# Kernel optimization log

Hardware: AMD Instinct MI355X
Metric: run time of the kernel (lower is better)

## Reference

```python
import jax, jax.numpy as jnp
import numpy as np

# dims
S = 8192       # total ragged tokens
B = 8          # number of sequences
L = 1024       # tokens per sequence (equal-length ragged batch)
HID = 2048     # hidden_size
H = 16         # num_attention_heads
KV = 4         # num_key_value_heads (GQA)
D = 128        # head_dim
HALF = D // 2
MAXPOS = 1024  # rope table length
MROPE_SECTION = [16, 24, 24]  # sums to HALF
SCALE = (1.0 / D) ** 0.5      # module default: sqrt(1/head_dim)
THETA = 1_000_000.0


def setup_inputs() -> dict:
    key = jax.random.key(0)
    ks = jax.random.split(key, 9)
    x = jax.random.normal(ks[0], (S, HID), jnp.float32)
    # torch-style Linear weights: [out_dim, in_dim]
    wq = jax.random.normal(ks[1], (H * D, HID), jnp.float32) * 0.02
    wk = jax.random.normal(ks[2], (KV * D, HID), jnp.float32) * 0.02
    wv = jax.random.normal(ks[3], (KV * D, HID), jnp.float32) * 0.02
    bq = jax.random.normal(ks[4], (H * D,), jnp.float32) * 0.02
    bk = jax.random.normal(ks[5], (KV * D,), jnp.float32) * 0.02
    bv = jax.random.normal(ks[6], (KV * D,), jnp.float32) * 0.02
    wo = jax.random.normal(ks[7], (HID, H * D), jnp.float32) * 0.02
    # rope table: freqs_cis[p, f] = (cos(p*inv_freq[f]), sin(p*inv_freq[f]))
    inv_freq = 1.0 / (THETA ** (jnp.arange(0, HALF, dtype=jnp.float32) / HALF))
    freqs = jnp.arange(MAXPOS, dtype=jnp.float32)[:, None] * inv_freq[None, :]
    freqs_cis = jnp.stack([jnp.cos(freqs), jnp.sin(freqs)], axis=-1)  # [MAXPOS, HALF, 2]
    # multi-axis (t/h/w) position ids, one row per mrope axis
    position_ids = jnp.tile(jnp.arange(L, dtype=jnp.int32), B)[None, :].repeat(3, axis=0)  # [3, S]
    input_row_offsets = jnp.arange(B + 1, dtype=jnp.int32) * L  # ragged offsets
    return {"x": x, "wq": wq, "wk": wk, "wv": wv, "bq": bq, "bk": bk, "bv": bv,
            "wo": wo, "freqs_cis": freqs_cis, "position_ids": position_ids,
            "input_row_offsets": input_row_offsets}


def _mrope_cos_sin(freqs_cis, position_ids):
    # gather per-axis cos/sin then select mrope sections along the freq dim
    cs = freqs_cis[position_ids]           # [3, S, HALF, 2]
    bounds = np.cumsum([0] + MROPE_SECTION)
    sel = jnp.concatenate([cs[i, :, bounds[i]:bounds[i + 1], :] for i in range(3)], axis=1)  # [S, HALF, 2]
    cos = sel[:, None, :, 0]               # [S, 1, HALF] broadcast over heads
    sin = sel[:, None, :, 1]
    return cos, sin


def _rope(t, cos, sin):
    # non-interleaved (rotate-half) rope on last dim of size D
    t1, t2 = jnp.split(t, 2, axis=-1)
    return jnp.concatenate([t1 * cos - t2 * sin, t2 * cos + t1 * sin], axis=-1)


def reference(x, wq, wk, wv, bq, bk, bv, wo, freqs_cis, position_ids, input_row_offsets):
    # fused ragged QKV projection (wqkv = concat(wq, wk, wv) along out dim)
    wqkv = jnp.concatenate([wq, wk, wv], axis=0)          # [H*D + 2*KV*D, HID]
    bqkv = jnp.concatenate([bq, bk, bv], axis=0)
    qkv = x @ wqkv.T + bqkv                                # [S, H*D + 2*KV*D]
    q = qkv[:, :H * D].reshape(S, H, D)
    k = qkv[:, H * D:H * D + KV * D].reshape(S, KV, D)
    v = qkv[:, H * D + KV * D:].reshape(S, KV, D)
    # fused multi-axis rotary embedding on q and k
    cos, sin = _mrope_cos_sin(freqs_cis, position_ids)
    q = _rope(q, cos, sin)
    k = _rope(k, cos, sin)
    # ragged causal flash attention; sequences are equal length so reshape to
    # [B, L, ...] which honors the ragged structure given input_row_offsets = arange(B+1)*L
    qb = q.reshape(B, L, H, D)
    kb = jnp.repeat(k.reshape(B, L, KV, D), H // KV, axis=2)  # GQA expand
    vb = jnp.repeat(v.reshape(B, L, KV, D), H // KV, axis=2)
    scores = jnp.einsum('bqhd,bkhd->bhqk', qb, kb) * SCALE    # [B, H, L, L]
    causal = jnp.tril(jnp.ones((L, L), dtype=bool))
    scores = jnp.where(causal, scores, jnp.float32(-1e30))
    attn = jax.nn.softmax(scores, axis=-1)
    out = jnp.einsum('bhqk,bkhd->bqhd', attn, vb).reshape(S, H * D)
    return out @ wo.T                                         # [S, HID]
```

## Files before the change

### kernel.cpp

```cpp
#include <hip/hip_runtime.h>

#define S_TOK 8192
#define BATCH 8
#define LSEQ 1024
#define HID 2048
#define NH 16
#define NKV 4
#define DHEAD 128
#define QKV_W 3072
#define SCALE_F 0.08838834764831845f

typedef __attribute__((ext_vector_type(8))) unsigned short u16x8;
typedef __attribute__((ext_vector_type(8))) __bf16 bf16x8;
typedef __attribute__((ext_vector_type(4))) float f32x4;

__device__ __forceinline__ unsigned short f2bf(float f) {
  unsigned u = __builtin_bit_cast(unsigned, f);
  unsigned r = u + 0x7fffu + ((u >> 16) & 1u);
  return (unsigned short)(r >> 16);
}
__device__ __forceinline__ float bf2f(unsigned short h) {
  return __builtin_bit_cast(float, (unsigned)h << 16);
}

__device__ __forceinline__ void async16(const void* g, void* l) {
  __builtin_amdgcn_global_load_lds(
      (const __attribute__((address_space(1))) void*)g,
      (__attribute__((address_space(3))) void*)l, 16, 0, 0);
}

__global__ __launch_bounds__(256) void conv_f2b(const float* __restrict__ src,
                                                unsigned short* __restrict__ dst,
                                                int n8) {
  int t = blockIdx.x * 256 + threadIdx.x;
  if (t >= n8) return;
  const f32x4* s4 = (const f32x4*)(src + (size_t)t * 8);
  f32x4 v0 = s4[0], v1 = s4[1];
  u16x8 o;
#pragma unroll
  for (int j = 0; j < 4; ++j) { o[j] = f2bf(v0[j]); o[4 + j] = f2bf(v1[j]); }
  *(u16x8*)(dst + (size_t)t * 8) = o;
}

__global__ __launch_bounds__(256) void conv_w3(const float* __restrict__ wq,
                                               const float* __restrict__ wk,
                                               const float* __restrict__ wv,
                                               unsigned short* __restrict__ dst,
                                               int n8) {
  int t = blockIdx.x * 256 + threadIdx.x;
  if (t >= n8) return;
  size_t idx = (size_t)t * 8;
  int row = (int)(idx >> 11);
  int col = (int)(idx & 2047);
  const float* src;
  if (row < 2048)      src = wq + ((size_t)row << 11) + col;
  else if (row < 2560) src = wk + ((size_t)(row - 2048) << 11) + col;
  else                 src = wv + ((size_t)(row - 2560) << 11) + col;
  const f32x4* s4 = (const f32x4*)src;
  f32x4 v0 = s4[0], v1 = s4[1];
  u16x8 o;
#pragma unroll
  for (int j = 0; j < 4; ++j) { o[j] = f2bf(v0[j]); o[4 + j] = f2bf(v1[j]); }
  *(u16x8*)(dst + idx) = o;
}

template <bool ADD_BIAS, bool OUT_BF16>
__global__ __launch_bounds__(256) void gemm_bt(const unsigned short* __restrict__ A,
                                               const unsigned short* __restrict__ Bw,
                                               const float* __restrict__ bias,
                                               void* __restrict__ Cout,
                                               int M, int N, int K) {
  __shared__ unsigned short A_lds[128 * 32];
  __shared__ unsigned short B_lds[128 * 32];
  const int tid = threadIdx.x;
  const int w = tid >> 6, lane = tid & 63;
  const int lr = lane & 15, lg = lane >> 4;
  const int wr = w >> 1, wc = w & 1;
  const int m0 = blockIdx.y * 128, n0 = blockIdx.x * 128;

  f32x4 acc[4][4];
#pragma unroll
  for (int mi = 0; mi < 4; ++mi)
#pragma unroll
    for (int nj = 0; nj < 4; ++nj) acc[mi][nj] = (f32x4){0.f, 0.f, 0.f, 0.f};

  const int nk = K >> 5;
  const int srow = (lane >> 2);
  const int scol = (lane & 3) * 8;
  for (int kt = 0; kt < nk; ++kt) {
#pragma unroll
    for (int q = 0; q < 2; ++q) {
      int chunk = w * 2 + q;
      int row = chunk * 16 + srow;
      async16(A + (size_t)(m0 + row) * K + kt * 32 + scol, &A_lds[chunk * 512]);
      async16(Bw + (size_t)(n0 + row) * K + kt * 32 + scol, &B_lds[chunk * 512]);
    }
    __syncthreads();
    bf16x8 a[4], bb[4];
#pragma unroll
    for (int mi = 0; mi < 4; ++mi)
      a[mi] = *(const bf16x8*)&A_lds[(wr * 64 + mi * 16 + lr) * 32 + lg * 8];
#pragma unroll
    for (int nj = 0; nj < 4; ++nj)
      bb[nj] = *(const bf16x8*)&B_lds[(wc * 64 + nj * 16 + lr) * 32 + lg * 8];
#pragma unroll
    for (int mi = 0; mi < 4; ++mi)
#pragma unroll
      for (int nj = 0; nj < 4; ++nj)
        acc[mi][nj] = __builtin_amdgcn_mfma_f32_16x16x32_bf16(a[mi], bb[nj], acc[mi][nj], 0, 0, 0);
    __syncthreads();
  }

#pragma unroll
  for (int mi = 0; mi < 4; ++mi)
#pragma unroll
    for (int nj = 0; nj < 4; ++nj)
#pragma unroll
      for (int j = 0; j < 4; ++j) {
        int row = m0 + wr * 64 + mi * 16 + lg * 4 + j;
        int col = n0 + wc * 64 + nj * 16 + lr;
        float v = acc[mi][nj][j];
        if (ADD_BIAS) v += bias[col];
        if (OUT_BF16)
          ((unsigned short*)Cout)[(size_t)row * N + col] = f2bf(v);
        else
          ((float*)Cout)[(size_t)row * N + col] = v;
      }
}

__global__ __launch_bounds__(256) void rope_k(unsigned short* __restrict__ qkv,
                                              const float* __restrict__ fc,
                                              const int* __restrict__ pid) {
  int t = blockIdx.x * 256 + threadIdx.x;
  int j0 = (t & 7) << 3;
  int hh = (t >> 3) % 20;
  int s = t / 160;
  if (s >= S_TOK) return;
  int sec = (j0 < 16) ? 0 : (j0 < 40 ? 1 : 2);
  int pos = pid[sec * S_TOK + s];
  const float* cs = fc + ((size_t)pos * 64 + j0) * 2;
  unsigned short* p = qkv + (size_t)s * QKV_W + hh * 128 + j0;
  u16x8 t1 = *(const u16x8*)p;
  u16x8 t2 = *(const u16x8*)(p + 64);
  u16x8 o1, o2;
#pragma unroll
  for (int j = 0; j < 8; ++j) {
    float c = cs[2 * j], sn = cs[2 * j + 1];
    float x1 = bf2f(t1[j]), x2 = bf2f(t2[j]);
    o1[j] = f2bf(x1 * c - x2 * sn);
    o2[j] = f2bf(x2 * c + x1 * sn);
  }
  *(u16x8*)p = o1;
  *(u16x8*)(p + 64) = o2;
}

__global__ __launch_bounds__(256) void attn_fwd(const unsigned short* __restrict__ qkv,
                                                unsigned short* __restrict__ aout) {
  __shared__ unsigned short K_lds[64 * 128];
  __shared__ unsigned short V_T[128 * 64];
  __shared__ unsigned short P_lds[4 * 32 * 64];
  char* Kb = (char*)K_lds;
  char* Vb = (char*)V_T;
  char* Pb = (char*)P_lds;
  const int tid = threadIdx.x, w = tid >> 6, lane = tid & 63;
  const int lr = lane & 15, lg = lane >> 4;
  const int q0 = blockIdx.x * 128, h = blockIdx.y, b = blockIdx.z, kvh = h >> 2;

  bf16x8 qf[2][4];
#pragma unroll
  for (int mi = 0; mi < 2; ++mi)
#pragma unroll
    for (int kk = 0; kk < 4; ++kk)
      qf[mi][kk] = *(const bf16x8*)(qkv + (size_t)(b * LSEQ + q0 + w * 32 + mi * 16 + lr) * QKV_W +
                                    h * 128 + kk * 32 + lg * 8);

  f32x4 o[2][8];
#pragma unroll
  for (int mi = 0; mi < 2; ++mi)
#pragma unroll
    for (int nj = 0; nj < 8; ++nj) o[mi][nj] = (f32x4){0.f, 0.f, 0.f, 0.f};
  float m_run[2][4], l_run[2][4];
#pragma unroll
  for (int mi = 0; mi < 2; ++mi)
#pragma unroll
    for (int j = 0; j < 4; ++j) { m_run[mi][j] = -1e30f; l_run[mi][j] = 0.f; }

  const int ntiles = (q0 >> 6) + 2;
  for (int kt = 0; kt < ntiles; ++kt) {
    const int k0 = kt * 64;
#pragma unroll
    for (int c4 = 0; c4 < 4; ++c4) {
      int chunk = w * 4 + c4;
      int row = chunk * 4 + lg;
      int colE = (lr * 8) ^ ((row & 7) * 8);
      async16(qkv + (size_t)(b * LSEQ + k0 + row) * QKV_W + HID + kvh * 128 + colE,
              &K_lds[chunk * 512]);
    }
#pragma unroll
    for (int r = 0; r < 4; ++r) {
      int d0 = (r * 4 + w) * 8;
      u16x8 vv = *(const u16x8*)(qkv + (size_t)(b * LSEQ + k0 + lane) * QKV_W + HID + NKV * 128 +
                                 kvh * 128 + d0);
#pragma unroll
      for (int j = 0; j < 8; ++j)
        *(unsigned short*)(Vb + (d0 + j) * 128 + ((lane * 2) ^ (j << 4))) = vv[j];
    }
    __syncthreads();

    f32x4 s[2][4];
#pragma unroll
    for (int mi = 0; mi < 2; ++mi)
#pragma unroll
      for (int nj = 0; nj < 4; ++nj) s[mi][nj] = (f32x4){0.f, 0.f, 0.f, 0.f};
#pragma unroll
    for (int kk = 0; kk < 4; ++kk) {
#pragma unroll
      for (int nj = 0; nj < 4; ++nj) {
        bf16x8 kb = *(const bf16x8*)(Kb + (nj * 16 + lr) * 256 +
                                     ((kk * 64 + lg * 16) ^ ((lr & 7) << 4)));
        s[0][nj] = __builtin_amdgcn_mfma_f32_16x16x32_bf16(qf[0][kk], kb, s[0][nj], 0, 0, 0);
        s[1][nj] = __builtin_amdgcn_mfma_f32_16x16x32_bf16(qf[1][kk], kb, s[1][nj], 0, 0, 0);
      }
    }

    float sf[2][4];
#pragma unroll
    for (int mi = 0; mi < 2; ++mi) {
#pragma unroll
      for (int j = 0; j < 4; ++j) {
        int qg = q0 + w * 32 + mi * 16 + lg * 4 + j;
        float rm = -1e30f;
#pragma unroll
        for (int nj = 0; nj < 4; ++nj) {
          int kg = k0 + nj * 16 + lr;
          float v = s[mi][nj][j] * SCALE_F;
          v = (kg > qg) ? -1e30f : v;
          s[mi][nj][j] = v;
          rm = fmaxf(rm, v);
        }
        rm = fmaxf(rm, __shfl_xor(rm, 1, 64));
        rm = fmaxf(rm, __shfl_xor(rm, 2, 64));
        rm = fmaxf(rm, __shfl_xor(rm, 4, 64));
        rm = fmaxf(rm, __shfl_xor(rm, 8, 64));
        float mn = fmaxf(m_run[mi][j], rm);
        float sc = __expf(m_run[mi][j] - mn);
        m_run[mi][j] = mn;
        float rs = 0.f;
#pragma unroll
        for (int nj = 0; nj < 4; ++nj) {
          float p = __expf(s[mi][nj][j] - mn);
          s[mi][nj][j] = p;
          rs += p;
        }
        rs += __shfl_xor(rs, 1, 64);
        rs += __shfl_xor(rs, 2, 64);
        rs += __shfl_xor(rs, 4, 64);
        rs += __shfl_xor(rs, 8, 64);
        l_run[mi][j] = l_run[mi][j] * sc + rs;
        sf[mi][j] = sc;
      }
    }
#pragma unroll
    for (int mi = 0; mi < 2; ++mi)
#pragma unroll
      for (int nj = 0; nj < 8; ++nj)
#pragma unroll
        for (int j = 0; j < 4; ++j) o[mi][nj][j] *= sf[mi][j];
#pragma unroll
    for (int mi = 0; mi < 2; ++mi)
#pragma unroll
      for (int nj = 0; nj < 4; ++nj)
#pragma unroll
        for (int j = 0; j < 4; ++j) {
          int prow = mi * 16 + lg * 4 + j;
          *(unsigned short*)(Pb + w * 4096 + prow * 128 +
                             (((nj * 16 + lr) * 2) ^ ((prow & 7) << 4))) = f2bf(s[mi][nj][j]);
        }

#pragma unroll
    for (int kk2 = 0; kk2 < 2; ++kk2) {
      bf16x8 pa[2];
      pa[0] = *(const bf16x8*)(Pb + w * 4096 + lr * 128 +
                               ((kk2 * 64 + lg * 16) ^ ((lr & 7) << 4)));
      pa[1] = *(const bf16x8*)(Pb + w * 4096 + (16 + lr) * 128 +
                               ((kk2 * 64 + lg * 16) ^ ((lr & 7) << 4)));
#pragma unroll
      for (int nj = 0; nj < 8; ++nj) {
        bf16x8 vb = *(const bf16x8*)(Vb + (nj * 16 + lr) * 128 +
                                     ((kk2 * 64 + lg * 16) ^ ((lr & 7) << 4)));
        o[0][nj] = __builtin_amdgcn_mfma_f32_16x16x32_bf16(pa[0], vb, o[0][nj], 0, 0, 0);
        o[1][nj] = __builtin_amdgcn_mfma_f32_16x16x32_bf16(pa[1], vb, o[1][nj], 0, 0, 0);
      }
    }
    __syncthreads();
  }

#pragma unroll
  for (int mi = 0; mi < 2; ++mi)
#pragma unroll
    for (int j = 0; j < 4; ++j) {
      float inv = 1.0f / l_run[mi][j];
      int row = b * LSEQ + q0 + w * 32 + mi * 16 + lg * 4 + j;
#pragma unroll
      for (int nj = 0; nj < 8; ++nj)
        aout[(size_t)row * 2048 + h * 128 + nj * 16 + lr] = f2bf(o[mi][nj][j] * inv);
    }
}

extern "C" void kernel_launch(void* const* d_in, const int* in_sizes, int n_in,
                              void* d_out, int out_size, void* d_ws, size_t ws_size,
                              hipStream_t stream) {
  const float* x = (const float*)d_in[0];
  const float* wq = (const float*)d_in[1];
  const float* wk = (const float*)d_in[2];
  const float* wv = (const float*)d_in[3];
  const float* bq = (const float*)d_in[4];
  const float* bk = (const float*)d_in[5];
  const float* bv = (const float*)d_in[6];
  const float* wo = (const float*)d_in[7];
  const float* fc = (const float*)d_in[8];
  const int* pid = (const int*)d_in[9];

  char* ws = (char*)d_ws;
  unsigned short* xb = (unsigned short*)ws;
  unsigned short* wqkvb = (unsigned short*)(ws + 33554432);
  unsigned short* wob = (unsigned short*)(ws + 46137344);
  float* bqkv = (float*)(ws + 54525952);
  unsigned short* qkv = (unsigned short*)(ws + 54538240);
  unsigned short* aout = xb;

  hipMemcpyAsync(bqkv, bq, 2048 * 4, hipMemcpyDeviceToDevice, stream);
  hipMemcpyAsync(bqkv + 2048, bk, 512 * 4, hipMemcpyDeviceToDevice, stream);
  hipMemcpyAsync(bqkv + 2560, bv, 512 * 4, hipMemcpyDeviceToDevice, stream);

  conv_f2b<<<8192, 256, 0, stream>>>(x, xb, 2097152);
  conv_w3<<<3072, 256, 0, stream>>>(wq, wk, wv, wqkvb, 786432);
  conv_f2b<<<2048, 256, 0, stream>>>(wo, wob, 524288);

  gemm_bt<true, true><<<dim3(24, 64), 256, 0, stream>>>(xb, wqkvb, bqkv, qkv, 8192, 3072, 2048);
  rope_k<<<5120, 256, 0, stream>>>(qkv, fc, pid);
  attn_fwd<<<dim3(8, 16, 8), 256, 0, stream>>>(qkv, aout);
  gemm_bt<false, false><<<dim3(16, 64), 256, 0, stream>>>(aout, wob, nullptr, d_out, 8192, 2048, 2048);
}
```

Baseline: 662.3 us.

## Double-buffer K/V tiles in attention and schedule longest query blocks first

The attention kernel now keeps two LDS buffers for K and V. The next tile's K is issued as an async copy, and its V is loaded into registers before the current tile's QK^T and PV MFMAs run, so global latency overlaps compute and one barrier per iteration is dropped. The V transpose write to the other buffer happens after the PV step. Query blocks are also traversed in reverse order, so the heaviest causal blocks launch first for better load balance. This doubles K/V LDS use (about 80KB per block), which may cut occupancy, and holds extra V registers.

New measurement: 700.5 us. 1.06x slower.

```diff
diff --git a/kernel.cpp b/kernel.cpp
--- a/kernel.cpp
+++ b/kernel.cpp
@@ -156,15 +156,45 @@
 
 __global__ __launch_bounds__(256) void attn_fwd(const unsigned short* __restrict__ qkv,
                                                 unsigned short* __restrict__ aout) {
-  __shared__ unsigned short K_lds[64 * 128];
-  __shared__ unsigned short V_T[128 * 64];
-  __shared__ unsigned short P_lds[4 * 32 * 64];
-  char* Kb = (char*)K_lds;
-  char* Vb = (char*)V_T;
+  __shared__ unsigned short K_lds[2][8192];
+  __shared__ unsigned short V_T[2][8192];
+  __shared__ unsigned short P_lds[4 * 2048];
   char* Pb = (char*)P_lds;
   const int tid = threadIdx.x, w = tid >> 6, lane = tid & 63;
   const int lr = lane & 15, lg = lane >> 4;
-  const int q0 = blockIdx.x * 128, h = blockIdx.y, b = blockIdx.z, kvh = h >> 2;
+  const int q0 = (7 - (int)blockIdx.x) * 128;
+  const int h = blockIdx.y, b = blockIdx.z, kvh = h >> 2;
+  const size_t kvbase = (size_t)(b * LSEQ) * QKV_W;
+
+#define STAGE_K(bf, k0_)                                                                   \
+  {                                                                                        \
+    _Pragma("unroll") for (int c4 = 0; c4 < 4; ++c4) {                                     \
+      int c = w * 4 + c4;                                                                  \
+      int row = c * 4 + lg;                                                                \
+      int colE = (lr * 8) ^ ((row & 7) * 8);                                               \
+      async16(qkv + kvbase + (size_t)((k0_) + row) * QKV_W + HID + kvh * 128 + colE,       \
+              &K_lds[bf][c * 512]);                                                        \
+    }                                                                                      \
+  }
+
+#define LOAD_V(k0_)                                                                        \
+  {                                                                                        \
+    _Pragma("unroll") for (int r = 0; r < 4; ++r) {                                        \
+      int d0 = (r * 4 + w) * 8;                                                            \
+      vreg[r] = *(const u16x8*)(qkv + kvbase + (size_t)((k0_) + lane) * QKV_W + HID +      \
+                                NKV * 128 + kvh * 128 + d0);                               \
+    }                                                                                      \
+  }
+
+#define WRITE_V(bf)                                                                        \
+  {                                                                                        \
+    char* Vb_ = (char*)&V_T[bf][0];                                                        \
+    _Pragma("unroll") for (int r = 0; r < 4; ++r) {                                        \
+      int d0 = (r * 4 + w) * 8;                                                            \
+      _Pragma("unroll") for (int j = 0; j < 8; ++j)                                        \
+          *(unsigned short*)(Vb_ + (d0 + j) * 128 + ((lane * 2) ^ (j << 4))) = vreg[r][j]; \
+    }                                                                                      \
+  }
 
   bf16x8 qf[2][4];
 #pragma unroll
@@ -185,28 +215,23 @@
 #pragma unroll
     for (int j = 0; j < 4; ++j) { m_run[mi][j] = -1e30f; l_run[mi][j] = 0.f; }
 
+  u16x8 vreg[4];
+  STAGE_K(0, 0);
+  LOAD_V(0);
+  WRITE_V(0);
+  __syncthreads();
+
   const int ntiles = (q0 >> 6) + 2;
   for (int kt = 0; kt < ntiles; ++kt) {
+    const int cb = kt & 1;
     const int k0 = kt * 64;
-#pragma unroll
-    for (int c4 = 0; c4 < 4; ++c4) {
-      int chunk = w * 4 + c4;
-      int row = chunk * 4 + lg;
-      int colE = (lr * 8) ^ ((row & 7) * 8);
-      async16(qkv + (size_t)(b * LSEQ + k0 + row) * QKV_W + HID + kvh * 128 + colE,
-              &K_lds[chunk * 512]);
-    }
-#pragma unroll
-    for (int r = 0; r < 4; ++r) {
-      int d0 = (r * 4 + w) * 8;
-      u16x8 vv = *(const u16x8*)(qkv + (size_t)(b * LSEQ + k0 + lane) * QKV_W + HID + NKV * 128 +
-                                 kvh * 128 + d0);
-#pragma unroll
-      for (int j = 0; j < 8; ++j)
-        *(unsigned short*)(Vb + (d0 + j) * 128 + ((lane * 2) ^ (j << 4))) = vv[j];
-    }
-    __syncthreads();
-
+    const bool more = (kt + 1 < ntiles);
+    if (more) {
+      STAGE_K(cb ^ 1, k0 + 64);
+      LOAD_V(k0 + 64);
+    }
+
+    char* Kb = (char*)&K_lds[cb][0];
     f32x4 s[2][4];
 #pragma unroll
     for (int mi = 0; mi < 2; ++mi)
@@ -277,21 +302,25 @@
                              (((nj * 16 + lr) * 2) ^ ((prow & 7) << 4))) = f2bf(s[mi][nj][j]);
         }
 
-#pragma unroll
-    for (int kk2 = 0; kk2 < 2; ++kk2) {
-      bf16x8 pa[2];
-      pa[0] = *(const bf16x8*)(Pb + w * 4096 + lr * 128 +
-                               ((kk2 * 64 + lg * 16) ^ ((lr & 7) << 4)));
-      pa[1] = *(const bf16x8*)(Pb + w * 4096 + (16 + lr) * 128 +
-                               ((kk2 * 64 + lg * 16) ^ ((lr & 7) << 4)));
-#pragma unroll
-      for (int nj = 0; nj < 8; ++nj) {
-        bf16x8 vb = *(const bf16x8*)(Vb + (nj * 16 + lr) * 128 +
-                                     ((kk2 * 64 + lg * 16) ^ ((lr & 7) << 4)));
-        o[0][nj] = __builtin_amdgcn_mfma_f32_16x16x32_bf16(pa[0], vb, o[0][nj], 0, 0, 0);
-        o[1][nj] = __builtin_amdgcn_mfma_f32_16x16x32_bf16(pa[1], vb, o[1][nj], 0, 0, 0);
+    {
+      char* Vb = (char*)&V_T[cb][0];
+#pragma unroll
+      for (int kk2 = 0; kk2 < 2; ++kk2) {
+        bf16x8 pa0 = *(const bf16x8*)(Pb + w * 4096 + lr * 128 +
+                                      ((kk2 * 64 + lg * 16) ^ ((lr & 7) << 4)));
+        bf16x8 pa1 = *(const bf16x8*)(Pb + w * 4096 + (16 + lr) * 128 +
+                                      ((kk2 * 64 + lg * 16) ^ ((lr & 7) << 4)));
+#pragma unroll
+        for (int nj = 0; nj < 8; ++nj) {
+          bf16x8 vb = *(const bf16x8*)(Vb + (nj * 16 + lr) * 128 +
+                                       ((kk2 * 64 + lg * 16) ^ ((lr & 7) << 4)));
+          o[0][nj] = __builtin_amdgcn_mfma_f32_16x16x32_bf16(pa0, vb, o[0][nj], 0, 0, 0);
+          o[1][nj] = __builtin_amdgcn_mfma_f32_16x16x32_bf16(pa1, vb, o[1][nj], 0, 0, 0);
+        }
       }
     }
+
+    if (more) WRITE_V(cb ^ 1);
     __syncthreads();
   }
 
```

## Compute transposed S tiles to cut softmax shuffles, reverse block order, add setprio

Applied to the files above, without the earlier changes.

The QK^T MFMA now runs with K as the A operand, so each lane holds a column of scores for a single query row. Row max and sum then need two cross-lane shuffles per row group instead of four per element row, and each lane keeps one running max and sum per row tile. Query blocks are issued in reverse order so the longest causal blocks start first, which should help load balance. s_setprio is raised around the MFMA sections. The change adds shuffle broadcasts of the scale and sum back to the output layout, and the scattered stores of P into LDS are unchanged.

After: 622.3 us. 1.06x faster.

```diff
diff --git a/kernel.cpp b/kernel.cpp
--- a/kernel.cpp
+++ b/kernel.cpp
@@ -158,20 +158,22 @@
                                                 unsigned short* __restrict__ aout) {
   __shared__ unsigned short K_lds[64 * 128];
   __shared__ unsigned short V_T[128 * 64];
-  __shared__ unsigned short P_lds[4 * 32 * 64];
+  __shared__ unsigned short P_lds[4 * 2048];
   char* Kb = (char*)K_lds;
   char* Vb = (char*)V_T;
   char* Pb = (char*)P_lds;
   const int tid = threadIdx.x, w = tid >> 6, lane = tid & 63;
   const int lr = lane & 15, lg = lane >> 4;
-  const int q0 = blockIdx.x * 128, h = blockIdx.y, b = blockIdx.z, kvh = h >> 2;
+  const int q0 = (7 - (int)blockIdx.x) * 128;
+  const int h = blockIdx.y, b = blockIdx.z, kvh = h >> 2;
+  const size_t kvbase = (size_t)(b * LSEQ) * QKV_W;
 
   bf16x8 qf[2][4];
 #pragma unroll
   for (int mi = 0; mi < 2; ++mi)
 #pragma unroll
     for (int kk = 0; kk < 4; ++kk)
-      qf[mi][kk] = *(const bf16x8*)(qkv + (size_t)(b * LSEQ + q0 + w * 32 + mi * 16 + lr) * QKV_W +
+      qf[mi][kk] = *(const bf16x8*)(qkv + kvbase + (size_t)(q0 + w * 32 + mi * 16 + lr) * QKV_W +
                                     h * 128 + kk * 32 + lg * 8);
 
   f32x4 o[2][8];
@@ -179,11 +181,7 @@
   for (int mi = 0; mi < 2; ++mi)
 #pragma unroll
     for (int nj = 0; nj < 8; ++nj) o[mi][nj] = (f32x4){0.f, 0.f, 0.f, 0.f};
-  float m_run[2][4], l_run[2][4];
-#pragma unroll
-  for (int mi = 0; mi < 2; ++mi)
-#pragma unroll
-    for (int j = 0; j < 4; ++j) { m_run[mi][j] = -1e30f; l_run[mi][j] = 0.f; }
+  float m_run[2] = {-1e30f, -1e30f}, l_run[2] = {0.f, 0.f};
 
   const int ntiles = (q0 >> 6) + 2;
   for (int kt = 0; kt < ntiles; ++kt) {
@@ -193,13 +191,13 @@
       int chunk = w * 4 + c4;
       int row = chunk * 4 + lg;
       int colE = (lr * 8) ^ ((row & 7) * 8);
-      async16(qkv + (size_t)(b * LSEQ + k0 + row) * QKV_W + HID + kvh * 128 + colE,
+      async16(qkv + kvbase + (size_t)(k0 + row) * QKV_W + HID + kvh * 128 + colE,
               &K_lds[chunk * 512]);
     }
 #pragma unroll
     for (int r = 0; r < 4; ++r) {
       int d0 = (r * 4 + w) * 8;
-      u16x8 vv = *(const u16x8*)(qkv + (size_t)(b * LSEQ + k0 + lane) * QKV_W + HID + NKV * 128 +
+      u16x8 vv = *(const u16x8*)(qkv + kvbase + (size_t)(k0 + lane) * QKV_W + HID + NKV * 128 +
                                  kvh * 128 + d0);
 #pragma unroll
       for (int j = 0; j < 8; ++j)
@@ -207,99 +205,112 @@
     }
     __syncthreads();
 
-    f32x4 s[2][4];
-#pragma unroll
-    for (int mi = 0; mi < 2; ++mi)
-#pragma unroll
-      for (int nj = 0; nj < 4; ++nj) s[mi][nj] = (f32x4){0.f, 0.f, 0.f, 0.f};
+    f32x4 sT[4][2];
+#pragma unroll
+    for (int nj = 0; nj < 4; ++nj)
+#pragma unroll
+      for (int mi = 0; mi < 2; ++mi) sT[nj][mi] = (f32x4){0.f, 0.f, 0.f, 0.f};
+    __builtin_amdgcn_s_setprio(1);
 #pragma unroll
     for (int kk = 0; kk < 4; ++kk) {
 #pragma unroll
       for (int nj = 0; nj < 4; ++nj) {
         bf16x8 kb = *(const bf16x8*)(Kb + (nj * 16 + lr) * 256 +
                                      ((kk * 64 + lg * 16) ^ ((lr & 7) << 4)));
-        s[0][nj] = __builtin_amdgcn_mfma_f32_16x16x32_bf16(qf[0][kk], kb, s[0][nj], 0, 0, 0);
-        s[1][nj] = __builtin_amdgcn_mfma_f32_16x16x32_bf16(qf[1][kk], kb, s[1][nj], 0, 0, 0);
+        sT[nj][0] = __builtin_amdgcn_mfma_f32_16x16x32_bf16(kb, qf[0][kk], sT[nj][0], 0, 0, 0);
+        sT[nj][1] = __builtin_amdgcn_mfma_f32_16x16x32_bf16(kb, qf[1][kk], sT[nj][1], 0, 0, 0);
       }
     }
-
-    float sf[2][4];
+    __builtin_amdgcn_s_setprio(0);
+
+    float sc[2];
 #pragma unroll
     for (int mi = 0; mi < 2; ++mi) {
-#pragma unroll
-      for (int j = 0; j < 4; ++j) {
-        int qg = q0 + w * 32 + mi * 16 + lg * 4 + j;
-        float rm = -1e30f;
-#pragma unroll
-        for (int nj = 0; nj < 4; ++nj) {
-          int kg = k0 + nj * 16 + lr;
-          float v = s[mi][nj][j] * SCALE_F;
-          v = (kg > qg) ? -1e30f : v;
-          s[mi][nj][j] = v;
-          rm = fmaxf(rm, v);
+      int qg = q0 + w * 32 + mi * 16 + lr;
+      float vmax = -1e30f;
+#pragma unroll
+      for (int nj = 0; nj < 4; ++nj)
+#pragma unroll
+        for (int j = 0; j < 4; ++j) {
+          int kvg = k0 + nj * 16 + lg * 4 + j;
+          float v = sT[nj][mi][j] * SCALE_F;
+          v = (kvg > qg) ? -1e30f : v;
+          sT[nj][mi][j] = v;
+          vmax = fmaxf(vmax, v);
         }
-        rm = fmaxf(rm, __shfl_xor(rm, 1, 64));
-        rm = fmaxf(rm, __shfl_xor(rm, 2, 64));
-        rm = fmaxf(rm, __shfl_xor(rm, 4, 64));
-        rm = fmaxf(rm, __shfl_xor(rm, 8, 64));
-        float mn = fmaxf(m_run[mi][j], rm);
-        float sc = __expf(m_run[mi][j] - mn);
-        m_run[mi][j] = mn;
-        float rs = 0.f;
-#pragma unroll
-        for (int nj = 0; nj < 4; ++nj) {
-          float p = __expf(s[mi][nj][j] - mn);
-          s[mi][nj][j] = p;
+      vmax = fmaxf(vmax, __shfl_xor(vmax, 16, 64));
+      vmax = fmaxf(vmax, __shfl_xor(vmax, 32, 64));
+      float mn = fmaxf(m_run[mi], vmax);
+      sc[mi] = __expf(m_run[mi] - mn);
+      m_run[mi] = mn;
+      float rs = 0.f;
+#pragma unroll
+      for (int nj = 0; nj < 4; ++nj)
+#pragma unroll
+        for (int j = 0; j < 4; ++j) {
+          float p = __expf(sT[nj][mi][j] - mn);
+          sT[nj][mi][j] = p;
           rs += p;
         }
-        rs += __shfl_xor(rs, 1, 64);
-        rs += __shfl_xor(rs, 2, 64);
-        rs += __shfl_xor(rs, 4, 64);
-        rs += __shfl_xor(rs, 8, 64);
-        l_run[mi][j] = l_run[mi][j] * sc + rs;
-        sf[mi][j] = sc;
-      }
-    }
+      rs += __shfl_xor(rs, 16, 64);
+      rs += __shfl_xor(rs, 32, 64);
+      l_run[mi] = l_run[mi] * sc[mi] + rs;
+    }
+
+#pragma unroll
+    for (int mi = 0; mi < 2; ++mi) {
+      int prow = mi * 16 + lr;
+#pragma unroll
+      for (int nj = 0; nj < 4; ++nj)
+#pragma unroll
+        for (int j = 0; j < 4; ++j) {
+          int pcol = nj * 16 + lg * 4 + j;
+          *(unsigned short*)(Pb + w * 4096 + prow * 128 + ((pcol * 2) ^ ((prow & 7) << 4))) =
+              f2bf(sT[nj][mi][j]);
+        }
+    }
+
+    float sfb[2][4];
 #pragma unroll
     for (int mi = 0; mi < 2; ++mi)
 #pragma unroll
+      for (int j = 0; j < 4; ++j) sfb[mi][j] = __shfl(sc[mi], lg * 4 + j, 64);
+#pragma unroll
+    for (int mi = 0; mi < 2; ++mi)
+#pragma unroll
       for (int nj = 0; nj < 8; ++nj)
 #pragma unroll
-        for (int j = 0; j < 4; ++j) o[mi][nj][j] *= sf[mi][j];
-#pragma unroll
-    for (int mi = 0; mi < 2; ++mi)
-#pragma unroll
-      for (int nj = 0; nj < 4; ++nj)
-#pragma unroll
-        for (int j = 0; j < 4; ++j) {
-          int prow = mi * 16 + lg * 4 + j;
-          *(unsigned short*)(Pb + w * 4096 + prow * 128 +
-                             (((nj * 16 + lr) * 2) ^ ((prow & 7) << 4))) = f2bf(s[mi][nj][j]);
-        }
-
+        for (int j = 0; j < 4; ++j) o[mi][nj][j] *= sfb[mi][j];
+
+    __builtin_amdgcn_s_setprio(1);
 #pragma unroll
     for (int kk2 = 0; kk2 < 2; ++kk2) {
-      bf16x8 pa[2];
-      pa[0] = *(const bf16x8*)(Pb + w * 4096 + lr * 128 +
-                               ((kk2 * 64 + lg * 16) ^ ((lr & 7) << 4)));
-      pa[1] = *(const bf16x8*)(Pb + w * 4096 + (16 + lr) * 128 +
-                               ((kk2 * 64 + lg * 16) ^ ((lr & 7) << 4)));
+      bf16x8 pa0 = *(const bf16x8*)(Pb + w * 4096 + lr * 128 +
+                                    ((kk2 * 64 + lg * 16) ^ ((lr & 7) << 4)));
+      bf16x8 pa1 = *(const bf16x8*)(Pb + w * 4096 + (16 + lr) * 128 +
+                                    ((kk2 * 64 + lg * 16) ^ ((lr & 7) << 4)));
 #pragma unroll
       for (int nj = 0; nj < 8; ++nj) {
         bf16x8 vb = *(const bf16x8*)(Vb + (nj * 16 + lr) * 128 +
                                      ((kk2 * 64 + lg * 16) ^ ((lr & 7) << 4)));
-        o[0][nj] = __builtin_amdgcn_mfma_f32_16x16x32_bf16(pa[0], vb, o[0][nj], 0, 0, 0);
-        o[1][nj] = __builtin_amdgcn_mfma_f32_16x16x32_bf16(pa[1], vb, o[1][nj], 0, 0, 0);
+        o[0][nj] = __builtin_amdgcn_mfma_f32_16x16x32_bf16(pa0, vb, o[0][nj], 0, 0, 0);
+        o[1][nj] = __builtin_amdgcn_mfma_f32_16x16x32_bf16(pa1, vb, o[1][nj], 0, 0, 0);
       }
     }
+    __builtin_amdgcn_s_setprio(0);
     __syncthreads();
   }
 
+  float lb[2][4];
 #pragma unroll
   for (int mi = 0; mi < 2; ++mi)
 #pragma unroll
+    for (int j = 0; j < 4; ++j) lb[mi][j] = __shfl(l_run[mi], lg * 4 + j, 64);
+#pragma unroll
+  for (int mi = 0; mi < 2; ++mi)
+#pragma unroll
     for (int j = 0; j < 4; ++j) {
-      float inv = 1.0f / l_run[mi][j];
+      float inv = 1.0f / lb[mi][j];
       int row = b * LSEQ + q0 + w * 32 + mi * 16 + lg * 4 + j;
 #pragma unroll
       for (int nj = 0; nj < 8; ++nj)
```
